# Optimization experiments

Hardware: AMD Instinct MI355X
Metric: run time of the kernel (lower is better)

Reference implementation:

```python
import jax, jax.numpy as jnp
from jax import lax
import numpy as np
import math

IN_CH = 256
SCALES = [128, 256, 512]
ASPECT = [0.5, 1.0, 2.0]
NUM_A = len(SCALES) * len(ASPECT)  # 9
PRENMS_TOPK = 2000
RPN_TOPK = 1000
NMS_TH = 0.7
MIN_SIZE = 16.0
IMG_H = IMG_W = 1600
FEAT_H = FEAT_W = 200
BBOX_CLIP = math.log(1000.0 / 16.0)  # standard dw/dh clamp in box decoding


def setup_inputs() -> dict:
    key = jax.random.key(0)
    ks = jax.random.split(key, 6)
    image = jax.random.normal(ks[0], (1, 3, IMG_H, IMG_W), jnp.float32)
    feat = jax.random.normal(ks[1], (1, IN_CH, FEAT_H, FEAT_W), jnp.float32)
    # params init per init_weights(): normal(std=0.01), zero bias
    conv_w = jax.random.normal(ks[2], (IN_CH, IN_CH, 3, 3), jnp.float32) * 0.01
    conv_b = jnp.zeros((IN_CH,), jnp.float32)
    cls_w = jax.random.normal(ks[3], (NUM_A, IN_CH, 1, 1), jnp.float32) * 0.01
    cls_b = jnp.zeros((NUM_A,), jnp.float32)
    reg_w = jax.random.normal(ks[4], (NUM_A * 4, IN_CH, 1, 1), jnp.float32) * 0.01
    reg_b = jnp.zeros((NUM_A * 4,), jnp.float32)
    return dict(image=image, feat=feat, conv_w=conv_w, conv_b=conv_b,
                cls_w=cls_w, cls_b=cls_b, reg_w=reg_w, reg_b=reg_b)


def _conv(x, w, b, pad):
    y = lax.conv_general_dilated(x, w, (1, 1), [(pad, pad), (pad, pad)],
                                 dimension_numbers=('NCHW', 'OIHW', 'NCHW'))
    return y + b[None, :, None, None]


def _generate_anchors(img_hw, feat_hw):
    # static (numpy) anchor grid, faithful to generate_anchors_
    gh, gw = feat_hw
    ih, iw = img_hw
    sh, sw = ih // gh, iw // gw
    scales = np.array(SCALES, np.float32)
    ar = np.array(ASPECT, np.float32)
    hr = np.sqrt(ar)
    wr = 1.0 / hr
    ws = (wr[:, None] * scales[None, :]).reshape(-1)
    hs = (hr[:, None] * scales[None, :]).reshape(-1)
    base = np.round(np.stack([-ws, -hs, ws, hs], axis=1) / 2.0)  # (A,4)
    sx = np.arange(gw, dtype=np.float32) * sw
    sy = np.arange(gh, dtype=np.float32) * sh
    yy, xx = np.meshgrid(sy, sx, indexing='ij')
    xx = xx.reshape(-1)
    yy = yy.reshape(-1)
    shifts = np.stack([xx, yy, xx, yy], axis=1)  # (H*W,4)
    anchors = (shifts[:, None, :] + base[None, :, :]).reshape(-1, 4)
    return jnp.asarray(anchors, jnp.float32)


def _apply_deltas(anchors, deltas):
    w = anchors[:, 2] - anchors[:, 0]
    h = anchors[:, 3] - anchors[:, 1]
    cx = anchors[:, 0] + 0.5 * w
    cy = anchors[:, 1] + 0.5 * h
    dx, dy = deltas[:, 0], deltas[:, 1]
    dw = jnp.minimum(deltas[:, 2], BBOX_CLIP)
    dh = jnp.minimum(deltas[:, 3], BBOX_CLIP)
    pcx = dx * w + cx
    pcy = dy * h + cy
    pw = jnp.exp(dw) * w
    ph = jnp.exp(dh) * h
    return jnp.stack([pcx - 0.5 * pw, pcy - 0.5 * ph,
                      pcx + 0.5 * pw, pcy + 0.5 * ph], axis=1)


def _nms_keep(boxes, valid, thresh):
    # boxes sorted by descending score; greedy NMS via dense IoU matrix
    K = boxes.shape[0]
    area = (boxes[:, 2] - boxes[:, 0]) * (boxes[:, 3] - boxes[:, 1])
    lt = jnp.maximum(boxes[:, None, :2], boxes[None, :, :2])
    rb = jnp.minimum(boxes[:, None, 2:], boxes[None, :, 2:])
    wh = jnp.maximum(rb - lt, 0.0)
    inter = wh[..., 0] * wh[..., 1]
    iou = inter / (area[:, None] + area[None, :] - inter + 1e-9)
    idx = jnp.arange(K)

    def body(i, keep):
        sup = (iou[i] > thresh) & keep[i] & (idx > i)
        return keep & (~sup)

    return lax.fori_loop(0, K, body, valid)


def reference(image, feat, conv_w, conv_b, cls_w, cls_b, reg_w, reg_b):
    H, W = feat.shape[-2], feat.shape[-1]
    x = jax.nn.relu(_conv(feat, conv_w, conv_b, 1))          # (1,C,H,W)
    cls = _conv(x, cls_w, cls_b, 0)                          # (1,A,H,W)
    scores = cls.transpose(0, 2, 3, 1).reshape(-1)           # (H*W*A,)
    reg = _conv(x, reg_w, reg_b, 0)                          # (1,4A,H,W)
    deltas = reg.reshape(1, NUM_A, 4, H, W).transpose(0, 3, 4, 1, 2).reshape(-1, 4)
    anchors = _generate_anchors((image.shape[-2], image.shape[-1]), (H, W))
    proposals = _apply_deltas(anchors, lax.stop_gradient(deltas))  # .detach() in source

    s = jax.nn.sigmoid(scores)
    topv, topi = lax.top_k(s, PRENMS_TOPK)                   # sorted descending
    p = proposals[topi]
    ih = jnp.float32(image.shape[-2])
    iw = jnp.float32(image.shape[-1])
    p = jnp.stack([jnp.clip(p[:, 0], 0.0, iw), jnp.clip(p[:, 1], 0.0, ih),
                   jnp.clip(p[:, 2], 0.0, iw), jnp.clip(p[:, 3], 0.0, ih)], axis=1)
    valid = ((p[:, 2] - p[:, 0]) >= MIN_SIZE) & ((p[:, 3] - p[:, 1]) >= MIN_SIZE)
    sc = jnp.where(valid, topv, -1.0)                        # invalid -> score -1 (masked out)
    order = jnp.argsort(-sc)
    b = p[order]
    sc = sc[order]
    v = valid[order]
    keep = _nms_keep(b, v, NMS_TH)
    final = jnp.where(keep, sc, -1.0)
    fi = jnp.argsort(-final)[:RPN_TOPK]                      # post-NMS sort + topk
    sel = final[fi]
    out_boxes = jnp.where(sel[:, None] > 0.0, b[fi], 0.0)
    out_scores = jnp.where(sel > 0.0, sel, 0.0)
    return out_boxes, out_scores
```

## Files before the change

### kernel.cpp

```cpp
#include <hip/hip_runtime.h>
#include <math.h>

#define FH 200
#define FW 200
#define HW 40000
#define NUM_A 9
#define NANCH 360000
#define PRE_K 2000
#define OUT_K 1000
#define IMG_SZ 1600.0f
#define MIN_SZ 16.0f
#define NMS_TH 0.7f
#define BBOX_CLIP_F 4.135166556742356f

#define OFF_HIST   ((size_t)0)
#define OFF_STATE  ((size_t)1024)
#define OFF_CAND   ((size_t)1088)
#define OFF_BOXS   ((size_t)33856)
#define OFF_SCS    ((size_t)65856)
#define OFF_MASK   ((size_t)73856)
#define OFF_DIAG   ((size_t)585856)
#define OFF_AWH    ((size_t)602240)
#define OFF_AWM    ((size_t)1781888)
#define OFF_AWL    ((size_t)2961536)
#define OFF_HWH    ((size_t)4141184)
#define OFF_HWM    ((size_t)4165760)
#define OFF_HWL    ((size_t)4190336)
#define OFF_LOGIT  ((size_t)4214912)
#define OFF_PH     ((size_t)18614912)
#define OFF_PM     ((size_t)39094912)
#define OFF_PL     ((size_t)59574912)
#define OFF_PROP   ((size_t)18614912)
#define OFF_SCORE  ((size_t)24374912)

typedef __attribute__((ext_vector_type(8))) short short8;
typedef __attribute__((ext_vector_type(4))) float floatx4;
#define MFMA16(a, b, c) __builtin_amdgcn_mfma_f32_16x16x32_bf16(a, b, c, 0, 0, 0)

__device__ __forceinline__ unsigned short rne_bf16(float v) {
  unsigned int bb = __float_as_uint(v);
  return (unsigned short)((bb + 0x7FFFu + ((bb >> 16) & 1u)) >> 16);
}

__device__ __forceinline__ void split3(float v, unsigned short& h,
                                       unsigned short& m, unsigned short& l) {
  h = rne_bf16(v);
  float r1 = v - __uint_as_float(((unsigned int)h) << 16);
  m = rne_bf16(r1);
  float r2 = r1 - __uint_as_float(((unsigned int)m) << 16);
  l = rne_bf16(r2);
}

__global__ __launch_bounds__(256) void prep_weights(
    const float* __restrict__ w, const float* __restrict__ cls_w,
    const float* __restrict__ reg_w, uint4* __restrict__ AW_h,
    uint4* __restrict__ AW_m, uint4* __restrict__ AW_l,
    uint4* __restrict__ HwF_h, uint4* __restrict__ HwF_m,
    uint4* __restrict__ HwF_l) {
  int gid = blockIdx.x * 256 + threadIdx.x;
  unsigned short h[8], m[8], l[8];
  if (gid < 73728) {
    int L = gid & 63;
    int idx = gid >> 6;
    int cib = idx & 7;
    int tmp = idx >> 3;
    int tap = tmp % 9;
    int ctg = tmp / 9;
    int co = ctg * 16 + (L & 15);
    int ci0 = cib * 32 + (L >> 4) * 8;
#pragma unroll
    for (int j = 0; j < 8; ++j)
      split3(w[(size_t)co * 2304 + (ci0 + j) * 9 + tap], h[j], m[j], l[j]);
    uint4 vh, vm, vl;
    vh.x = h[0] | (h[1] << 16); vh.y = h[2] | (h[3] << 16);
    vh.z = h[4] | (h[5] << 16); vh.w = h[6] | (h[7] << 16);
    vm.x = m[0] | (m[1] << 16); vm.y = m[2] | (m[3] << 16);
    vm.z = m[4] | (m[5] << 16); vm.w = m[6] | (m[7] << 16);
    vl.x = l[0] | (l[1] << 16); vl.y = l[2] | (l[3] << 16);
    vl.z = l[4] | (l[5] << 16); vl.w = l[6] | (l[7] << 16);
    AW_h[gid] = vh; AW_m[gid] = vm; AW_l[gid] = vl;
  } else if (gid < 73728 + 1536) {
    int g2 = gid - 73728;
    int L = g2 & 63;
    int idx = g2 >> 6;
    int kb = idx & 7;
    int mt = idx >> 3;
    int mm = mt * 16 + (L & 15);
    int co0 = kb * 32 + (L >> 4) * 8;
#pragma unroll
    for (int j = 0; j < 8; ++j) {
      float v = 0.f;
      if (mm < 9) v = cls_w[mm * 256 + co0 + j];
      else if (mm < 45) v = reg_w[(mm - 9) * 256 + co0 + j];
      split3(v, h[j], m[j], l[j]);
    }
    uint4 vh, vm, vl;
    vh.x = h[0] | (h[1] << 16); vh.y = h[2] | (h[3] << 16);
    vh.z = h[4] | (h[5] << 16); vh.w = h[6] | (h[7] << 16);
    vm.x = m[0] | (m[1] << 16); vm.y = m[2] | (m[3] << 16);
    vm.z = m[4] | (m[5] << 16); vm.w = m[6] | (m[7] << 16);
    vl.x = l[0] | (l[1] << 16); vl.y = l[2] | (l[3] << 16);
    vl.z = l[4] | (l[5] << 16); vl.w = l[6] | (l[7] << 16);
    HwF_h[g2] = vh; HwF_m[g2] = vm; HwF_l[g2] = vl;
  }
}

__global__ __launch_bounds__(256) void prep_feat(
    const float* __restrict__ feat, unsigned short* __restrict__ Ph,
    unsigned short* __restrict__ Pm, unsigned short* __restrict__ Pl) {
  int px = blockIdx.x * 256 + threadIdx.x;
  int cib = blockIdx.y;
  if (px >= HW) return;
  unsigned short h[32], m[32], l[32];
#pragma unroll
  for (int ci = 0; ci < 32; ++ci)
    split3(feat[(size_t)(cib * 32 + ci) * HW + px], h[ci], m[ci], l[ci]);
  size_t base = ((size_t)cib * HW + px) * 32;
  uint4* dh = (uint4*)(Ph + base);
  uint4* dm = (uint4*)(Pm + base);
  uint4* dl = (uint4*)(Pl + base);
#pragma unroll
  for (int k = 0; k < 4; ++k) {
    uint4 vh, vm, vl;
    vh.x = h[k * 8 + 0] | (h[k * 8 + 1] << 16);
    vh.y = h[k * 8 + 2] | (h[k * 8 + 3] << 16);
    vh.z = h[k * 8 + 4] | (h[k * 8 + 5] << 16);
    vh.w = h[k * 8 + 6] | (h[k * 8 + 7] << 16);
    vm.x = m[k * 8 + 0] | (m[k * 8 + 1] << 16);
    vm.y = m[k * 8 + 2] | (m[k * 8 + 3] << 16);
    vm.z = m[k * 8 + 4] | (m[k * 8 + 5] << 16);
    vm.w = m[k * 8 + 6] | (m[k * 8 + 7] << 16);
    vl.x = l[k * 8 + 0] | (l[k * 8 + 1] << 16);
    vl.y = l[k * 8 + 2] | (l[k * 8 + 3] << 16);
    vl.z = l[k * 8 + 4] | (l[k * 8 + 5] << 16);
    vl.w = l[k * 8 + 6] | (l[k * 8 + 7] << 16);
    dh[k] = vh; dm[k] = vm; dl[k] = vl;
  }
}

__global__ __launch_bounds__(256) void conv_mfma(
    const unsigned short* __restrict__ Ph, const unsigned short* __restrict__ Pm,
    const unsigned short* __restrict__ Pl, const uint4* __restrict__ AW_h,
    const uint4* __restrict__ AW_m, const uint4* __restrict__ AW_l,
    const uint4* __restrict__ HwF_h, const uint4* __restrict__ HwF_m,
    const uint4* __restrict__ HwF_l, const float* __restrict__ bias,
    float* __restrict__ logits) {
  __shared__ alignas(16) unsigned short smem[26112];
  const int t = threadIdx.x;
  const int L = t & 63, wv = t >> 6;
  const int q = L >> 4, nl = L & 15;
  const int w0 = blockIdx.x * 16;
  const int h0 = blockIdx.y * 8;
  const int cb = blockIdx.z;

  floatx4 acc[2][8];
#pragma unroll
  for (int ct = 0; ct < 2; ++ct)
#pragma unroll
    for (int r = 0; r < 8; ++r) acc[ct][r] = (floatx4)0.f;

  unsigned short* flh = smem;
  unsigned short* flm = smem + 5760;
  unsigned short* fll = smem + 11520;

  for (int cib = 0; cib < 8; ++cib) {
    __syncthreads();
#pragma unroll
    for (int j = 0; j < 9; ++j) {
      const int p = j / 3;
      const int c = (j % 3) * 256 + t;
      if (c < 720) {
        int rr = (int)((unsigned)c / 72u);
        int rem = c - rr * 72;
        int cc = rem >> 2, q16 = rem & 3;
        int gr = h0 - 1 + rr, gc = w0 - 1 + cc;
        uint4 v; v.x = v.y = v.z = v.w = 0u;
        if ((unsigned)gr < (unsigned)FH && (unsigned)gc < (unsigned)FW) {
          const unsigned short* pp = (p == 0) ? Ph : (p == 1) ? Pm : Pl;
          v = *(const uint4*)(pp +
                ((size_t)(cib * HW + gr * FW + gc) * 32 + q16 * 8));
        }
        *(uint4*)(smem + p * 5760 + c * 8) = v;
      }
    }
    __syncthreads();
    const int ctg0 = cb * 8 + wv * 2;
    for (int kh = 0; kh < 3; ++kh) {
      for (int kw = 0; kw < 3; ++kw) {
        const int tap = kh * 3 + kw;
        const int abase = ((ctg0 * 9 + tap) * 8 + cib) * 64 + L;
        const int abase1 = abase + 9 * 8 * 64;
        short8 ah0 = ((const short8*)AW_h)[abase];
        short8 am0 = ((const short8*)AW_m)[abase];
        short8 al0 = ((const short8*)AW_l)[abase];
        short8 ah1 = ((const short8*)AW_h)[abase1];
        short8 am1 = ((const short8*)AW_m)[abase1];
        short8 al1 = ((const short8*)AW_l)[abase1];
        const int cbase = (nl + kw) * 32 + q * 8;
#pragma unroll
        for (int r = 0; r < 8; ++r) {
          const int off = (r + kh) * 576 + cbase;
          short8 bh = *(const short8*)(flh + off);
          short8 bm = *(const short8*)(flm + off);
          short8 bl = *(const short8*)(fll + off);
          acc[0][r] = MFMA16(ah0, bh, acc[0][r]);
          acc[0][r] = MFMA16(ah0, bm, acc[0][r]);
          acc[0][r] = MFMA16(am0, bh, acc[0][r]);
          acc[0][r] = MFMA16(ah0, bl, acc[0][r]);
          acc[0][r] = MFMA16(am0, bm, acc[0][r]);
          acc[0][r] = MFMA16(al0, bh, acc[0][r]);
          acc[1][r] = MFMA16(ah1, bh, acc[1][r]);
          acc[1][r] = MFMA16(ah1, bm, acc[1][r]);
          acc[1][r] = MFMA16(am1, bh, acc[1][r]);
          acc[1][r] = MFMA16(ah1, bl, acc[1][r]);
          acc[1][r] = MFMA16(am1, bm, acc[1][r]);
          acc[1][r] = MFMA16(al1, bh, acc[1][r]);
        }
      }
    }
  }

  float bv[2][4];
#pragma unroll
  for (int ct = 0; ct < 2; ++ct)
#pragma unroll
    for (int i = 0; i < 4; ++i)
      bv[ct][i] = bias[cb * 128 + (wv * 2 + ct) * 16 + q * 4 + i];

  unsigned short* xlh = smem;
  unsigned short* xlm = smem + 8704;
  unsigned short* xll = smem + 17408;

  for (int hp = 0; hp < 2; ++hp) {
    __syncthreads();
#pragma unroll
    for (int ct = 0; ct < 2; ++ct) {
#pragma unroll
      for (int rr = 0; rr < 4; ++rr) {
        int r = hp * 4 + rr;
        unsigned short xh[4], xm[4], xl_[4];
#pragma unroll
        for (int i = 0; i < 4; ++i) {
          float xv = fmaxf(acc[ct][r][i] + bv[ct][i], 0.f);
          split3(xv, xh[i], xm[i], xl_[i]);
        }
        int px_l = rr * 16 + nl;
        int co_l = (wv * 2 + ct) * 16 + q * 4;
        uint2 ph, pm, pl;
        ph.x = xh[0] | (xh[1] << 16); ph.y = xh[2] | (xh[3] << 16);
        pm.x = xm[0] | (xm[1] << 16); pm.y = xm[2] | (xm[3] << 16);
        pl.x = xl_[0] | (xl_[1] << 16); pl.y = xl_[2] | (xl_[3] << 16);
        *(uint2*)(xlh + px_l * 136 + co_l) = ph;
        *(uint2*)(xlm + px_l * 136 + co_l) = pm;
        *(uint2*)(xll + px_l * 136 + co_l) = pl;
      }
    }
    __syncthreads();
    floatx4 ha[3];
#pragma unroll
    for (int mt = 0; mt < 3; ++mt) ha[mt] = (floatx4)0.f;
    for (int ks = 0; ks < 4; ++ks) {
      const int off = (wv * 16 + nl) * 136 + ks * 32 + q * 8;
      short8 bh = *(const short8*)(xlh + off);
      short8 bm = *(const short8*)(xlm + off);
      short8 bl = *(const short8*)(xll + off);
#pragma unroll
      for (int mt = 0; mt < 3; ++mt) {
        const int hb = (mt * 8 + cb * 4 + ks) * 64 + L;
        short8 hh = ((const short8*)HwF_h)[hb];
        short8 hm = ((const short8*)HwF_m)[hb];
        short8 hl = ((const short8*)HwF_l)[hb];
        ha[mt] = MFMA16(hh, bh, ha[mt]);
        ha[mt] = MFMA16(hh, bm, ha[mt]);
        ha[mt] = MFMA16(hm, bh, ha[mt]);
        ha[mt] = MFMA16(hh, bl, ha[mt]);
        ha[mt] = MFMA16(hm, bm, ha[mt]);
        ha[mt] = MFMA16(hl, bh, ha[mt]);
      }
    }
    int gr = h0 + hp * 4 + wv;
    int gc = w0 + nl;
    if (gc < FW) {
      float* lp = logits + ((size_t)cb * HW + (size_t)(gr * FW + gc)) * 45;
#pragma unroll
      for (int mt = 0; mt < 3; ++mt)
#pragma unroll
        for (int i = 0; i < 4; ++i) {
          int head = mt * 16 + q * 4 + i;
          if (head < 45) lp[head] = ha[mt][i];
        }
    }
  }
}

__global__ __launch_bounds__(256) void finalize_kernel(
    const float* __restrict__ logits, const float* __restrict__ cls_b,
    const float* __restrict__ reg_b, float* __restrict__ prop,
    float* __restrict__ score) {
  int px = blockIdx.x * 256 + threadIdx.x;
  if (px >= HW) return;
  float A[45];
  const float* lpA = logits + (size_t)px * 45;
  const float* lpB = logits + (size_t)HW * 45 + (size_t)px * 45;
#pragma unroll
  for (int i = 0; i < 45; ++i) A[i] = lpA[i] + lpB[i];
  const float scv[3] = {128.f, 256.f, 512.f};
  const float arv[3] = {0.5f, 1.f, 2.f};
  float sx = (float)(px % FW) * 8.0f;
  float sy = (float)(px / FW) * 8.0f;
#pragma unroll
  for (int a = 0; a < NUM_A; ++a) {
    int ai = a / 3, si = a % 3;
    float hr = sqrtf(arv[ai]);
    float wr = 1.0f / hr;
    float rw = nearbyintf(wr * scv[si] * 0.5f);
    float rh = nearbyintf(hr * scv[si] * 0.5f);
    float ax0 = sx - rw, ay0 = sy - rh, ax1 = sx + rw, ay1 = sy + rh;
    float aw = ax1 - ax0, ah = ay1 - ay0;
    float cx = ax0 + 0.5f * aw, cy = ay0 + 0.5f * ah;
    float dx = A[9 + a * 4 + 0] + reg_b[a * 4 + 0];
    float dy = A[9 + a * 4 + 1] + reg_b[a * 4 + 1];
    float dw = fminf(A[9 + a * 4 + 2] + reg_b[a * 4 + 2], BBOX_CLIP_F);
    float dh = fminf(A[9 + a * 4 + 3] + reg_b[a * 4 + 3], BBOX_CLIP_F);
    float pcx = dx * aw + cx;
    float pcy = dy * ah + cy;
    float pw = expf(dw) * aw;
    float ph = expf(dh) * ah;
    size_t base = (size_t)(px * NUM_A + a) * 4;
    prop[base + 0] = pcx - 0.5f * pw;
    prop[base + 1] = pcy - 0.5f * ph;
    prop[base + 2] = pcx + 0.5f * pw;
    prop[base + 3] = pcy + 0.5f * ph;
    float lg = A[a] + cls_b[a];
    score[px * NUM_A + a] = 1.0f / (1.0f + expf(-lg));
  }
}

__global__ __launch_bounds__(256) void hist_kernel(
    const float* __restrict__ score, unsigned int* __restrict__ hist,
    const unsigned int* __restrict__ state, int pass) {
  __shared__ unsigned int h[256];
  int t = threadIdx.x;
  h[t] = 0;
  __syncthreads();
  unsigned int prefix = (pass == 0) ? 0u : state[0];
  int shift = 24 - 8 * pass;
  for (int i = blockIdx.x * 256 + t; i < NANCH; i += gridDim.x * 256) {
    unsigned int key = __float_as_uint(score[i]);
    bool m = (pass == 0) || ((key >> (32 - 8 * pass)) == prefix);
    if (m) atomicAdd(&h[(key >> shift) & 255u], 1u);
  }
  __syncthreads();
  if (h[t]) atomicAdd(&hist[t], h[t]);
}

__global__ __launch_bounds__(256) void scan_kernel(
    unsigned int* __restrict__ hist, unsigned int* __restrict__ state, int pass) {
  __shared__ unsigned int s0[256], s1[256];
  int t = threadIdx.x;
  unsigned int hv = hist[t];
  hist[t] = 0u;
  s0[t] = hv;
  __syncthreads();
  unsigned int* A = s0;
  unsigned int* B = s1;
  for (int off = 1; off < 256; off <<= 1) {
    B[t] = A[t] + ((t + off < 256) ? A[t + off] : 0u);
    __syncthreads();
    unsigned int* tmp = A; A = B; B = tmp;
  }
  unsigned int prefix = (pass == 0) ? 0u : state[0];
  unsigned int rem = (pass == 0) ? (unsigned)PRE_K : state[1];
  unsigned int suf = A[t];
  unsigned int sufn = (t < 255) ? A[t + 1] : 0u;
  if (suf >= rem && sufn < rem) {
    state[0] = (prefix << 8) | (unsigned int)t;
    state[1] = rem - sufn;
  }
}

__global__ __launch_bounds__(256) void collect_kernel(
    const float* __restrict__ score, unsigned int* __restrict__ state,
    unsigned long long* __restrict__ cand) {
  unsigned int T = state[0];
  for (int i = blockIdx.x * 256 + threadIdx.x; i < NANCH; i += gridDim.x * 256) {
    unsigned int key = __float_as_uint(score[i]);
    if (key >= T) {
      unsigned int pos = atomicAdd(&state[4], 1u);
      if (pos < 4096u)
        cand[pos] = ((unsigned long long)key << 32) |
                    (unsigned long long)(~(unsigned int)i);
    }
  }
}

__global__ __launch_bounds__(1024) void sort_gather(
    const unsigned long long* __restrict__ cand,
    const unsigned int* __restrict__ state, const float* __restrict__ prop,
    const float* __restrict__ score, float* __restrict__ boxes_s,
    float* __restrict__ sc_s) {
  __shared__ unsigned long long sk[4096];
  int t = threadIdx.x;
  unsigned int cnt = state[4];
  if (cnt > 4096u) cnt = 4096u;
  for (int e = t; e < 4096; e += 1024) sk[e] = (e < (int)cnt) ? cand[e] : 0ull;
  __syncthreads();
  for (int k = 2; k <= 4096; k <<= 1) {
    for (int j = k >> 1; j > 0; j >>= 1) {
      for (int i = t; i < 4096; i += 1024) {
        int l = i ^ j;
        if (l > i) {
          unsigned long long a = sk[i], bb = sk[l];
          bool up = ((i & k) == 0);
          bool sw = up ? (a < bb) : (a > bb);
          if (sw) { sk[i] = bb; sk[l] = a; }
        }
      }
      __syncthreads();
    }
  }
  float bx[2][4];
  float sc2[2] = {-1.f, -1.f};
  bool valid2[2] = {false, false};
#pragma unroll
  for (int s = 0; s < 2; ++s) {
    int i = t + s * 1024;
    bx[s][0] = bx[s][1] = bx[s][2] = bx[s][3] = 0.f;
    if (i < PRE_K) {
      unsigned long long v = sk[i];
      unsigned int idx = ~(unsigned int)(v & 0xFFFFFFFFull);
      float4 p = *(const float4*)(prop + (size_t)idx * 4);
      float x0 = fminf(fmaxf(p.x, 0.f), IMG_SZ);
      float y0 = fminf(fmaxf(p.y, 0.f), IMG_SZ);
      float x1 = fminf(fmaxf(p.z, 0.f), IMG_SZ);
      float y1 = fminf(fmaxf(p.w, 0.f), IMG_SZ);
      bool valid = (x1 - x0 >= MIN_SZ) && (y1 - y0 >= MIN_SZ);
      bx[s][0] = x0; bx[s][1] = y0; bx[s][2] = x1; bx[s][3] = y1;
      valid2[s] = valid;
      sc2[s] = valid ? score[idx] : -1.0f;
    }
  }
  __syncthreads();
  int* A = (int*)sk;
  int* B = A + 2048;
#pragma unroll
  for (int s = 0; s < 2; ++s) {
    int i = t + s * 1024;
    A[i] = (i < PRE_K && valid2[s]) ? 1 : 0;
  }
  __syncthreads();
  for (int off = 1; off < 2048; off <<= 1) {
#pragma unroll
    for (int s = 0; s < 2; ++s) {
      int i = t + s * 1024;
      B[i] = A[i] + ((i >= off) ? A[i - off] : 0);
    }
    __syncthreads();
    int* tmp = A; A = B; B = tmp;
  }
  int total = A[2047];
#pragma unroll
  for (int s = 0; s < 2; ++s) {
    int i = t + s * 1024;
    if (i < PRE_K) {
      int inc = A[i];
      int pos = valid2[s] ? (inc - 1) : (total + (i - inc));
      boxes_s[pos * 4 + 0] = bx[s][0];
      boxes_s[pos * 4 + 1] = bx[s][1];
      boxes_s[pos * 4 + 2] = bx[s][2];
      boxes_s[pos * 4 + 3] = bx[s][3];
      sc_s[pos] = sc2[s];
    }
  }
}

__global__ __launch_bounds__(64) void iou_kernel(
    const float* __restrict__ boxes_s, unsigned long long* __restrict__ mask,
    unsigned long long* __restrict__ diag) {
  int bi = blockIdx.y, bj = blockIdx.x;
  int t = threadIdx.x;
  __shared__ float4 cb[64];
  int jc = bj * 64 + t;
  float4 z; z.x = z.y = z.z = z.w = 0.f;
  cb[t] = (jc < PRE_K) ? *(const float4*)(boxes_s + (size_t)jc * 4) : z;
  __syncthreads();
  int i = bi * 64 + t;
  if (i >= PRE_K) return;
  float4 a = *(const float4*)(boxes_s + (size_t)i * 4);
  float areaA = (a.z - a.x) * (a.w - a.y);
  unsigned long long bits = 0ull;
  for (int jj = 0; jj < 64; ++jj) {
    int j = bj * 64 + jj;
    if (j < PRE_K && j > i) {
      float4 b = cb[jj];
      float areaB = (b.z - b.x) * (b.w - b.y);
      float ltx = fmaxf(a.x, b.x), lty = fmaxf(a.y, b.y);
      float rbx = fminf(a.z, b.z), rby = fminf(a.w, b.w);
      float w = fmaxf(rbx - ltx, 0.f), h = fmaxf(rby - lty, 0.f);
      float inter = w * h;
      float iou = inter / (areaA + areaB - inter + 1e-9f);
      if (iou > NMS_TH) bits |= (1ull << jj);
    }
  }
  mask[(size_t)i * 32 + bj] = bits;
  if (bi == bj) diag[i] = bits;
}

__global__ __launch_bounds__(256) void nms_out_kernel(
    const float* __restrict__ boxes_s, const float* __restrict__ sc_s,
    const unsigned long long* __restrict__ mask,
    const unsigned long long* __restrict__ diag, float* __restrict__ out) {
  int t = threadIdx.x;
  for (int e = t; e < (OUT_K * 4 + OUT_K); e += 256) out[e] = 0.f;
  __shared__ unsigned long long keepw[32];
  if (t < 64) {
    unsigned long long removed = 0ull;
    if (t < 32) {
      keepw[t] = 0ull;
#pragma unroll
      for (int k = 0; k < 64; ++k) {
        int idx = t * 64 + k;
        if (idx >= PRE_K || sc_s[idx] < 0.f) removed |= (1ull << k);
      }
    }
    const int w = t & 31;
    const int half = t >> 5;
    unsigned int kept = 0;
    for (int b = 0; b < 32; ++b) {
      unsigned long long d = diag[b * 64 + t];
      unsigned long long dead = __shfl(removed, b);
      unsigned long long alive = 0ull;
#pragma unroll
      for (int k = 0; k < 64; ++k) {
        unsigned long long dk = __shfl(d, k);
        if (!((dead >> k) & 1ull)) {
          alive |= (1ull << k);
          dead |= dk;
        }
      }
      if (t == 0) keepw[b] = alive;
      kept += (unsigned)__popcll(alive);
      if (kept >= (unsigned)OUT_K || b == 31) break;
      unsigned long long am = alive;
      const long long rb = (long long)b * 64;
      while (am) {
        int k0 = __ffsll(am) - 1; am &= am - 1;
        int k1 = k0, k2 = k0, k3 = k0, k4 = k0, k5 = k0, k6 = k0, k7 = k0;
        if (am) { k1 = __ffsll(am) - 1; am &= am - 1; }
        if (am) { k2 = __ffsll(am) - 1; am &= am - 1; }
        if (am) { k3 = __ffsll(am) - 1; am &= am - 1; }
        if (am) { k4 = __ffsll(am) - 1; am &= am - 1; }
        if (am) { k5 = __ffsll(am) - 1; am &= am - 1; }
        if (am) { k6 = __ffsll(am) - 1; am &= am - 1; }
        if (am) { k7 = __ffsll(am) - 1; am &= am - 1; }
        unsigned long long v0 = mask[(size_t)(rb + (half ? k1 : k0)) * 32 + w];
        unsigned long long v1 = mask[(size_t)(rb + (half ? k3 : k2)) * 32 + w];
        unsigned long long v2 = mask[(size_t)(rb + (half ? k5 : k4)) * 32 + w];
        unsigned long long v3 = mask[(size_t)(rb + (half ? k7 : k6)) * 32 + w];
        unsigned long long vv = v0 | v1 | v2 | v3;
        unsigned long long hv = __shfl(vv, w + 32);
        if (t < 32) removed |= vv | hv;
      }
    }
  }
  __syncthreads();
  __shared__ unsigned int wbase[32];
  if (t == 0) {
    unsigned int s = 0;
    for (int k = 0; k < 32; ++k) {
      wbase[k] = s;
      s += (unsigned)__popcll(keepw[k]);
    }
  }
  __syncthreads();
  for (int i = t; i < PRE_K; i += 256) {
    unsigned long long w2 = keepw[i >> 6];
    if ((w2 >> (i & 63)) & 1ull) {
      unsigned int pos =
          wbase[i >> 6] +
          (unsigned)__popcll(w2 & ((1ull << (i & 63)) - 1ull));
      if (pos < OUT_K) {
        out[pos * 4 + 0] = boxes_s[i * 4 + 0];
        out[pos * 4 + 1] = boxes_s[i * 4 + 1];
        out[pos * 4 + 2] = boxes_s[i * 4 + 2];
        out[pos * 4 + 3] = boxes_s[i * 4 + 3];
        out[OUT_K * 4 + pos] = sc_s[i];
      }
    }
  }
}

extern "C" void kernel_launch(void* const* d_in, const int* in_sizes, int n_in,
                              void* d_out, int out_size, void* d_ws,
                              size_t ws_size, hipStream_t stream) {
  const float* feat = (const float*)d_in[1];
  const float* convw = (const float*)d_in[2];
  const float* convb = (const float*)d_in[3];
  const float* clsw = (const float*)d_in[4];
  const float* clsb = (const float*)d_in[5];
  const float* regw = (const float*)d_in[6];
  const float* regb = (const float*)d_in[7];

  char* ws = (char*)d_ws;
  unsigned int* hist = (unsigned int*)(ws + OFF_HIST);
  unsigned int* state = (unsigned int*)(ws + OFF_STATE);
  unsigned long long* cand = (unsigned long long*)(ws + OFF_CAND);
  float* boxes_s = (float*)(ws + OFF_BOXS);
  float* sc_s = (float*)(ws + OFF_SCS);
  unsigned long long* mask = (unsigned long long*)(ws + OFF_MASK);
  unsigned long long* diag = (unsigned long long*)(ws + OFF_DIAG);
  uint4* AW_h = (uint4*)(ws + OFF_AWH);
  uint4* AW_m = (uint4*)(ws + OFF_AWM);
  uint4* AW_l = (uint4*)(ws + OFF_AWL);
  uint4* HwF_h = (uint4*)(ws + OFF_HWH);
  uint4* HwF_m = (uint4*)(ws + OFF_HWM);
  uint4* HwF_l = (uint4*)(ws + OFF_HWL);
  float* logits = (float*)(ws + OFF_LOGIT);
  unsigned short* Ph = (unsigned short*)(ws + OFF_PH);
  unsigned short* Pm = (unsigned short*)(ws + OFF_PM);
  unsigned short* Pl = (unsigned short*)(ws + OFF_PL);
  float* prop = (float*)(ws + OFF_PROP);
  float* score = (float*)(ws + OFF_SCORE);
  float* out = (float*)d_out;

  hipMemsetAsync(ws, 0, OFF_STATE + 64, stream);

  prep_weights<<<294, 256, 0, stream>>>(convw, clsw, regw, AW_h, AW_m, AW_l,
                                        HwF_h, HwF_m, HwF_l);
  prep_feat<<<dim3(157, 8), 256, 0, stream>>>(feat, Ph, Pm, Pl);
  conv_mfma<<<dim3(13, 25, 2), 256, 0, stream>>>(Ph, Pm, Pl, AW_h, AW_m, AW_l,
                                                 HwF_h, HwF_m, HwF_l, convb,
                                                 logits);
  finalize_kernel<<<157, 256, 0, stream>>>(logits, clsb, regb, prop, score);
  for (int p = 0; p < 4; ++p) {
    hist_kernel<<<256, 256, 0, stream>>>(score, hist, state, p);
    scan_kernel<<<1, 256, 0, stream>>>(hist, state, p);
  }
  collect_kernel<<<256, 256, 0, stream>>>(score, state, cand);
  sort_gather<<<1, 1024, 0, stream>>>(cand, state, prop, score, boxes_s, sc_s);
  iou_kernel<<<dim3(32, 32), 64, 0, stream>>>(boxes_s, mask, diag);
  nms_out_kernel<<<1, 256, 0, stream>>>(boxes_s, sc_s, mask, diag, out);
}
```

Before: 660.1 us.

## Merge prep kernels, pad conv LDS rows, fuse first histogram pass into finalize

Merges the weight and feature bf16-split prep kernels into a single launch. Pads the conv shared-memory tile (40-element pixel stride, 720 per row) to cut LDS bank conflicts, and raises wave priority around the MFMA loop. Builds the first radix-select histogram pass inside finalize, which removes one hist_kernel launch and one full read of the scores. Shared memory use grows and finalize now does extra shared-memory atomics.

```diff
diff --git a/kernel.cpp b/kernel.cpp
--- a/kernel.cpp
+++ b/kernel.cpp
@@ -51,13 +51,48 @@
   l = rne_bf16(r2);
 }
 
-__global__ __launch_bounds__(256) void prep_weights(
-    const float* __restrict__ w, const float* __restrict__ cls_w,
-    const float* __restrict__ reg_w, uint4* __restrict__ AW_h,
+__global__ __launch_bounds__(256) void prep_all(
+    const float* __restrict__ feat, const float* __restrict__ w,
+    const float* __restrict__ cls_w, const float* __restrict__ reg_w,
+    unsigned short* __restrict__ Ph, unsigned short* __restrict__ Pm,
+    unsigned short* __restrict__ Pl, uint4* __restrict__ AW_h,
     uint4* __restrict__ AW_m, uint4* __restrict__ AW_l,
     uint4* __restrict__ HwF_h, uint4* __restrict__ HwF_m,
     uint4* __restrict__ HwF_l) {
-  int gid = blockIdx.x * 256 + threadIdx.x;
+  int bx = blockIdx.x;
+  int t = threadIdx.x;
+  if (bx < 1256) {
+    int cib = bx & 7;
+    int px = (bx >> 3) * 256 + t;
+    if (px >= HW) return;
+    unsigned short h[32], m[32], l[32];
+#pragma unroll
+    for (int ci = 0; ci < 32; ++ci)
+      split3(feat[(size_t)(cib * 32 + ci) * HW + px], h[ci], m[ci], l[ci]);
+    size_t base = ((size_t)cib * HW + px) * 32;
+    uint4* dh = (uint4*)(Ph + base);
+    uint4* dm = (uint4*)(Pm + base);
+    uint4* dl = (uint4*)(Pl + base);
+#pragma unroll
+    for (int k = 0; k < 4; ++k) {
+      uint4 vh, vm, vl;
+      vh.x = h[k * 8 + 0] | (h[k * 8 + 1] << 16);
+      vh.y = h[k * 8 + 2] | (h[k * 8 + 3] << 16);
+      vh.z = h[k * 8 + 4] | (h[k * 8 + 5] << 16);
+      vh.w = h[k * 8 + 6] | (h[k * 8 + 7] << 16);
+      vm.x = m[k * 8 + 0] | (m[k * 8 + 1] << 16);
+      vm.y = m[k * 8 + 2] | (m[k * 8 + 3] << 16);
+      vm.z = m[k * 8 + 4] | (m[k * 8 + 5] << 16);
+      vm.w = m[k * 8 + 6] | (m[k * 8 + 7] << 16);
+      vl.x = l[k * 8 + 0] | (l[k * 8 + 1] << 16);
+      vl.y = l[k * 8 + 2] | (l[k * 8 + 3] << 16);
+      vl.z = l[k * 8 + 4] | (l[k * 8 + 5] << 16);
+      vl.w = l[k * 8 + 6] | (l[k * 8 + 7] << 16);
+      dh[k] = vh; dm[k] = vm; dl[k] = vl;
+    }
+    return;
+  }
+  int gid = (bx - 1256) * 256 + t;
   unsigned short h[8], m[8], l[8];
   if (gid < 73728) {
     int L = gid & 63;
@@ -105,39 +140,6 @@
   }
 }
 
-__global__ __launch_bounds__(256) void prep_feat(
-    const float* __restrict__ feat, unsigned short* __restrict__ Ph,
-    unsigned short* __restrict__ Pm, unsigned short* __restrict__ Pl) {
-  int px = blockIdx.x * 256 + threadIdx.x;
-  int cib = blockIdx.y;
-  if (px >= HW) return;
-  unsigned short h[32], m[32], l[32];
-#pragma unroll
-  for (int ci = 0; ci < 32; ++ci)
-    split3(feat[(size_t)(cib * 32 + ci) * HW + px], h[ci], m[ci], l[ci]);
-  size_t base = ((size_t)cib * HW + px) * 32;
-  uint4* dh = (uint4*)(Ph + base);
-  uint4* dm = (uint4*)(Pm + base);
-  uint4* dl = (uint4*)(Pl + base);
-#pragma unroll
-  for (int k = 0; k < 4; ++k) {
-    uint4 vh, vm, vl;
-    vh.x = h[k * 8 + 0] | (h[k * 8 + 1] << 16);
-    vh.y = h[k * 8 + 2] | (h[k * 8 + 3] << 16);
-    vh.z = h[k * 8 + 4] | (h[k * 8 + 5] << 16);
-    vh.w = h[k * 8 + 6] | (h[k * 8 + 7] << 16);
-    vm.x = m[k * 8 + 0] | (m[k * 8 + 1] << 16);
-    vm.y = m[k * 8 + 2] | (m[k * 8 + 3] << 16);
-    vm.z = m[k * 8 + 4] | (m[k * 8 + 5] << 16);
-    vm.w = m[k * 8 + 6] | (m[k * 8 + 7] << 16);
-    vl.x = l[k * 8 + 0] | (l[k * 8 + 1] << 16);
-    vl.y = l[k * 8 + 2] | (l[k * 8 + 3] << 16);
-    vl.z = l[k * 8 + 4] | (l[k * 8 + 5] << 16);
-    vl.w = l[k * 8 + 6] | (l[k * 8 + 7] << 16);
-    dh[k] = vh; dm[k] = vm; dl[k] = vl;
-  }
-}
-
 __global__ __launch_bounds__(256) void conv_mfma(
     const unsigned short* __restrict__ Ph, const unsigned short* __restrict__ Pm,
     const unsigned short* __restrict__ Pl, const uint4* __restrict__ AW_h,
@@ -160,8 +162,8 @@
     for (int r = 0; r < 8; ++r) acc[ct][r] = (floatx4)0.f;
 
   unsigned short* flh = smem;
-  unsigned short* flm = smem + 5760;
-  unsigned short* fll = smem + 11520;
+  unsigned short* flm = smem + 7200;
+  unsigned short* fll = smem + 14400;
 
   for (int cib = 0; cib < 8; ++cib) {
     __syncthreads();
@@ -180,10 +182,11 @@
           v = *(const uint4*)(pp +
                 ((size_t)(cib * HW + gr * FW + gc) * 32 + q16 * 8));
         }
-        *(uint4*)(smem + p * 5760 + c * 8) = v;
+        *(uint4*)(smem + p * 7200 + rr * 720 + cc * 40 + q16 * 8) = v;
       }
     }
     __syncthreads();
+    __builtin_amdgcn_s_setprio(1);
     const int ctg0 = cb * 8 + wv * 2;
     for (int kh = 0; kh < 3; ++kh) {
       for (int kw = 0; kw < 3; ++kw) {
@@ -196,10 +199,10 @@
         short8 ah1 = ((const short8*)AW_h)[abase1];
         short8 am1 = ((const short8*)AW_m)[abase1];
         short8 al1 = ((const short8*)AW_l)[abase1];
-        const int cbase = (nl + kw) * 32 + q * 8;
+        const int cbase = (nl + kw) * 40 + q * 8;
 #pragma unroll
         for (int r = 0; r < 8; ++r) {
-          const int off = (r + kh) * 576 + cbase;
+          const int off = (r + kh) * 720 + cbase;
           short8 bh = *(const short8*)(flh + off);
           short8 bm = *(const short8*)(flm + off);
           short8 bl = *(const short8*)(fll + off);
@@ -218,6 +221,7 @@
         }
       }
     }
+    __builtin_amdgcn_s_setprio(0);
   }
 
   float bv[2][4];
@@ -296,44 +300,53 @@
 __global__ __launch_bounds__(256) void finalize_kernel(
     const float* __restrict__ logits, const float* __restrict__ cls_b,
     const float* __restrict__ reg_b, float* __restrict__ prop,
-    float* __restrict__ score) {
-  int px = blockIdx.x * 256 + threadIdx.x;
-  if (px >= HW) return;
-  float A[45];
-  const float* lpA = logits + (size_t)px * 45;
-  const float* lpB = logits + (size_t)HW * 45 + (size_t)px * 45;
-#pragma unroll
-  for (int i = 0; i < 45; ++i) A[i] = lpA[i] + lpB[i];
-  const float scv[3] = {128.f, 256.f, 512.f};
-  const float arv[3] = {0.5f, 1.f, 2.f};
-  float sx = (float)(px % FW) * 8.0f;
-  float sy = (float)(px / FW) * 8.0f;
-#pragma unroll
-  for (int a = 0; a < NUM_A; ++a) {
-    int ai = a / 3, si = a % 3;
-    float hr = sqrtf(arv[ai]);
-    float wr = 1.0f / hr;
-    float rw = nearbyintf(wr * scv[si] * 0.5f);
-    float rh = nearbyintf(hr * scv[si] * 0.5f);
-    float ax0 = sx - rw, ay0 = sy - rh, ax1 = sx + rw, ay1 = sy + rh;
-    float aw = ax1 - ax0, ah = ay1 - ay0;
-    float cx = ax0 + 0.5f * aw, cy = ay0 + 0.5f * ah;
-    float dx = A[9 + a * 4 + 0] + reg_b[a * 4 + 0];
-    float dy = A[9 + a * 4 + 1] + reg_b[a * 4 + 1];
-    float dw = fminf(A[9 + a * 4 + 2] + reg_b[a * 4 + 2], BBOX_CLIP_F);
-    float dh = fminf(A[9 + a * 4 + 3] + reg_b[a * 4 + 3], BBOX_CLIP_F);
-    float pcx = dx * aw + cx;
-    float pcy = dy * ah + cy;
-    float pw = expf(dw) * aw;
-    float ph = expf(dh) * ah;
-    size_t base = (size_t)(px * NUM_A + a) * 4;
-    prop[base + 0] = pcx - 0.5f * pw;
-    prop[base + 1] = pcy - 0.5f * ph;
-    prop[base + 2] = pcx + 0.5f * pw;
-    prop[base + 3] = pcy + 0.5f * ph;
-    float lg = A[a] + cls_b[a];
-    score[px * NUM_A + a] = 1.0f / (1.0f + expf(-lg));
-  }
+    float* __restrict__ score, unsigned int* __restrict__ hist) {
+  __shared__ unsigned int hsh[256];
+  int t = threadIdx.x;
+  hsh[t] = 0u;
+  __syncthreads();
+  int px = blockIdx.x * 256 + t;
+  if (px < HW) {
+    float A[45];
+    const float* lpA = logits + (size_t)px * 45;
+    const float* lpB = logits + (size_t)HW * 45 + (size_t)px * 45;
+#pragma unroll
+    for (int i = 0; i < 45; ++i) A[i] = lpA[i] + lpB[i];
+    const float scv[3] = {128.f, 256.f, 512.f};
+    const float arv[3] = {0.5f, 1.f, 2.f};
+    float sx = (float)(px % FW) * 8.0f;
+    float sy = (float)(px / FW) * 8.0f;
+#pragma unroll
+    for (int a = 0; a < NUM_A; ++a) {
+      int ai = a / 3, si = a % 3;
+      float hr = sqrtf(arv[ai]);
+      float wr = 1.0f / hr;
+      float rw = nearbyintf(wr * scv[si] * 0.5f);
+      float rh = nearbyintf(hr * scv[si] * 0.5f);
+      float ax0 = sx - rw, ay0 = sy - rh, ax1 = sx + rw, ay1 = sy + rh;
+      float aw = ax1 - ax0, ah = ay1 - ay0;
+      float cx = ax0 + 0.5f * aw, cy = ay0 + 0.5f * ah;
+      float dx = A[9 + a * 4 + 0] + reg_b[a * 4 + 0];
+      float dy = A[9 + a * 4 + 1] + reg_b[a * 4 + 1];
+      float dw = fminf(A[9 + a * 4 + 2] + reg_b[a * 4 + 2], BBOX_CLIP_F);
+      float dh = fminf(A[9 + a * 4 + 3] + reg_b[a * 4 + 3], BBOX_CLIP_F);
+      float pcx = dx * aw + cx;
+      float pcy = dy * ah + cy;
+      float pw = expf(dw) * aw;
+      float ph = expf(dh) * ah;
+      size_t base = (size_t)(px * NUM_A + a) * 4;
+      prop[base + 0] = pcx - 0.5f * pw;
+      prop[base + 1] = pcy - 0.5f * ph;
+      prop[base + 2] = pcx + 0.5f * pw;
+      prop[base + 3] = pcy + 0.5f * ph;
+      float lg = A[a] + cls_b[a];
+      float sv = 1.0f / (1.0f + expf(-lg));
+      score[px * NUM_A + a] = sv;
+      atomicAdd(&hsh[__float_as_uint(sv) >> 24], 1u);
+    }
+  }
+  __syncthreads();
+  if (hsh[t]) atomicAdd(&hist[t], hsh[t]);
 }
 
 __global__ __launch_bounds__(256) void hist_kernel(
@@ -343,11 +356,11 @@
   int t = threadIdx.x;
   h[t] = 0;
   __syncthreads();
-  unsigned int prefix = (pass == 0) ? 0u : state[0];
+  unsigned int prefix = state[0];
   int shift = 24 - 8 * pass;
   for (int i = blockIdx.x * 256 + t; i < NANCH; i += gridDim.x * 256) {
     unsigned int key = __float_as_uint(score[i]);
-    bool m = (pass == 0) || ((key >> (32 - 8 * pass)) == prefix);
+    bool m = ((key >> (32 - 8 * pass)) == prefix);
     if (m) atomicAdd(&h[(key >> shift) & 255u], 1u);
   }
   __syncthreads();
@@ -625,14 +638,15 @@
 
   hipMemsetAsync(ws, 0, OFF_STATE + 64, stream);
 
-  prep_weights<<<294, 256, 0, stream>>>(convw, clsw, regw, AW_h, AW_m, AW_l,
-                                        HwF_h, HwF_m, HwF_l);
-  prep_feat<<<dim3(157, 8), 256, 0, stream>>>(feat, Ph, Pm, Pl);
+  prep_all<<<1550, 256, 0, stream>>>(feat, convw, clsw, regw, Ph, Pm, Pl,
+                                     AW_h, AW_m, AW_l, HwF_h, HwF_m, HwF_l);
   conv_mfma<<<dim3(13, 25, 2), 256, 0, stream>>>(Ph, Pm, Pl, AW_h, AW_m, AW_l,
                                                  HwF_h, HwF_m, HwF_l, convb,
                                                  logits);
-  finalize_kernel<<<157, 256, 0, stream>>>(logits, clsb, regb, prop, score);
-  for (int p = 0; p < 4; ++p) {
+  finalize_kernel<<<157, 256, 0, stream>>>(logits, clsb, regb, prop, score,
+                                           hist);
+  scan_kernel<<<1, 256, 0, stream>>>(hist, state, 0);
+  for (int p = 1; p < 4; ++p) {
     hist_kernel<<<256, 256, 0, stream>>>(score, hist, state, p);
     scan_kernel<<<1, 256, 0, stream>>>(hist, state, p);
   }
```

New measurement: 635.9 us. -3.7%, faster.
